# Kernel tuning notes

Measured on AMD Instinct MI355X. Metric: run time of the kernel, lower is better.

Reference implementation:

```python
import jax, jax.numpy as jnp
import numpy as np

BSZ, L, D = 64, 128, 2048


def setup_inputs() -> dict:
    key = jax.random.key(0)
    k1, k2, k3 = jax.random.split(key, 3)
    encoder_output = jax.random.normal(k1, (BSZ, L, D), dtype=jnp.float32)
    # ragged turn lengths in [2, L]; prefix mask like torch turn_lengths = mask.sum(1)
    lengths = jax.random.randint(k2, (BSZ,), 2, L + 1)
    mask = (jnp.arange(L)[None, :] < lengths[:, None]).astype(jnp.int32)
    W = jax.random.normal(k3, (2 * D, 2), dtype=jnp.float32) * (1.0 / np.sqrt(2 * D))
    b = jnp.zeros((2,), dtype=jnp.float32)
    return {"encoder_output": encoder_output, "mask": mask, "W": W, "b": b}


def reference(encoder_output, mask, W, b):
    bsz, max_len, d = encoder_output.shape
    turn_lengths = jnp.sum(mask, axis=1)  # [bsz]
    # con_fc(concat(h_j, h_k)) == h_j @ W[:d] + h_k @ W[d:] + b  (exact split of the linear)
    left = jnp.einsum('bld,dc->blc', encoder_output, W[:d])   # [b, L, 2]
    right = jnp.einsum('bld,dc->blc', encoder_output, W[d:])  # [b, L, 2]
    logits = left[:, :, None, :] + right[:, None, :, :] + b   # [b, L(j), L(k), 2]
    j = jnp.arange(max_len)[:, None]
    k = jnp.arange(max_len)[None, :]
    # pairs gathered by torch loops: k < j < turn_lengths[i]; label 1 iff k == j-1
    valid = (k < j) & (j < turn_lengths[:, None, None])        # [b, L, L]
    labels = (k == j - 1).astype(jnp.int32)                    # [L, L]
    logp = jax.nn.log_softmax(logits, axis=-1)                 # [b, L, L, 2]
    nll = -jnp.take_along_axis(
        logp, jnp.broadcast_to(labels[None, :, :, None], (bsz, max_len, max_len, 1)), axis=-1
    )[..., 0]                                                  # [b, L, L]
    n_valid = jnp.sum(valid)
    dli_loss = jnp.sum(jnp.where(valid, nll, 0.0)) / jnp.maximum(n_valid, 1).astype(nll.dtype)
    return dli_loss
```

## Files before the change

### kernel.cpp

```cpp
#include <hip/hip_runtime.h>

#define BSZ 64
#define LMAX 128
#define DIM 2048

struct Ctrl {
    float accum;
    int   count;
    int   done2;
};

__global__ __launch_bounds__(512) void proj_kernel(
        const float* __restrict__ enc,
        const float* __restrict__ W,
        float* __restrict__ proj,
        Ctrl* __restrict__ ctrl) {
    if (blockIdx.x == 0 && threadIdx.x == 0) {
        ctrl->accum = 0.0f;
        ctrl->count = 0;
        ctrl->done2 = 0;
    }

    __shared__ float4 sW[4][512];

    const float4* __restrict__ W4 = (const float4*)W;
    {
        const int i = threadIdx.x;
        sW[0][i] = W4[i * 2];
        sW[1][i] = W4[i * 2 + 1];
        sW[2][i] = W4[1024 + i * 2];
        sW[3][i] = W4[1024 + i * 2 + 1];
    }
    __syncthreads();

    const int wid  = threadIdx.x >> 6;
    const int lane = threadIdx.x & 63;
    const int p    = blockIdx.x * 8 + wid;

    const float4* __restrict__ h4 = (const float4*)(enc + (size_t)p * DIM);

    float a0 = 0.f, a1 = 0.f, a2 = 0.f, a3 = 0.f;
    #pragma unroll
    for (int it = 0; it < 8; ++it) {
        const int idx = it * 64 + lane;
        const float4 h  = h4[idx];
        const float4 w0 = sW[0][idx];
        const float4 w1 = sW[1][idx];
        const float4 w2 = sW[2][idx];
        const float4 w3 = sW[3][idx];
        a0 += h.x * w0.x + h.y * w0.z + h.z * w1.x + h.w * w1.z;
        a1 += h.x * w0.y + h.y * w0.w + h.z * w1.y + h.w * w1.w;
        a2 += h.x * w2.x + h.y * w2.z + h.z * w3.x + h.w * w3.z;
        a3 += h.x * w2.y + h.y * w2.w + h.z * w3.y + h.w * w3.w;
    }
    #pragma unroll
    for (int off = 32; off >= 1; off >>= 1) {
        a0 += __shfl_xor(a0, off);
        a1 += __shfl_xor(a1, off);
        a2 += __shfl_xor(a2, off);
        a3 += __shfl_xor(a3, off);
    }
    if (lane == 0) {
        float4 v; v.x = a0; v.y = a1; v.z = a2; v.w = a3;
        ((float4*)proj)[p] = v;
    }
}

__global__ __launch_bounds__(256) void loss_kernel(
        const int* __restrict__ mask,
        const float* __restrict__ proj,
        const float* __restrict__ bias,
        Ctrl* __restrict__ ctrl,
        float* __restrict__ out) {
    __shared__ float4 s_proj[LMAX];
    __shared__ float  s_w[4];
    __shared__ int    s_m[4];

    const int b   = blockIdx.x >> 2;
    const int q   = blockIdx.x & 3;
    const int tid = threadIdx.x;

    if (tid < LMAX) s_proj[tid] = ((const float4*)proj)[b * LMAX + tid];

    int m = (tid < LMAX) ? mask[b * LMAX + tid] : 0;
    #pragma unroll
    for (int off = 32; off >= 1; off >>= 1) m += __shfl_xor(m, off);
    if ((tid & 63) == 0) s_m[tid >> 6] = m;
    __syncthreads();

    const int   T  = s_m[0] + s_m[1] + s_m[2] + s_m[3];
    const float b0 = bias[0];
    const float b1 = bias[1];

    float local = 0.f;
    const int tmax = T << 7;
    for (int t = q * 256 + tid; t < tmax; t += 1024) {
        const int j = t >> 7;
        const int k = t & (LMAX - 1);
        if (k < j) {
            const float4 pj = s_proj[j];
            const float4 pk = s_proj[k];
            const float l0 = pj.x + pk.z + b0;
            const float l1 = pj.y + pk.w + b1;
            const bool  pos = (k == j - 1);
            const float d  = pos ? (l0 - l1) : (l1 - l0);
            local += fmaxf(d, 0.f) + __logf(1.f + __expf(-fabsf(d)));
        }
    }

    #pragma unroll
    for (int off = 32; off >= 1; off >>= 1) local += __shfl_xor(local, off);
    if ((tid & 63) == 0) s_w[tid >> 6] = local;
    __syncthreads();

    if (tid == 0) {
        atomicAdd(&ctrl->accum, s_w[0] + s_w[1] + s_w[2] + s_w[3]);
        if (q == 0) atomicAdd(&ctrl->count, T * (T - 1) / 2);
        __threadfence();
        const int prev = atomicAdd(&ctrl->done2, 1);
        if (prev == 4 * BSZ - 1) {
            const float s = atomicAdd(&ctrl->accum, 0.0f);
            const int   c = atomicAdd(&ctrl->count, 0);
            out[0] = s / (float)(c > 1 ? c : 1);
        }
    }
}

extern "C" void kernel_launch(void* const* d_in, const int* in_sizes, int n_in,
                              void* d_out, int out_size, void* d_ws, size_t ws_size,
                              hipStream_t stream) {
    const float* enc  = (const float*)d_in[0];
    const int*   mask = (const int*)d_in[1];
    const float* W    = (const float*)d_in[2];
    const float* bias = (const float*)d_in[3];
    float* out = (float*)d_out;

    float* proj = (float*)d_ws;
    Ctrl*  ctrl = (Ctrl*)((char*)d_ws + BSZ * LMAX * 16);

    proj_kernel<<<(BSZ * LMAX) / 8, 512, 0, stream>>>(enc, W, proj, ctrl);
    loss_kernel<<<4 * BSZ, 256, 0, stream>>>(mask, proj, bias, ctrl, out);
}
```

Before: 28.48 us.

## Keep W slices in registers, split rows across wave pairs, prefetch rows

The projection kernel no longer stages W in shared memory. Each wave holds half of W in registers and processes four consecutive rows, with the next row's loads issued before the current row's FMAs run. Each row is split across two waves that write separate partial results, which the loss kernel adds together. A transpose-style shuffle reduction is meant to cut shuffle count. In exchange the kernel uses more registers, launches half as many blocks, and needs twice the workspace for partials.

```diff
diff --git a/kernel.cpp b/kernel.cpp
--- a/kernel.cpp
+++ b/kernel.cpp
@@ -3,6 +3,7 @@
 #define BSZ 64
 #define LMAX 128
 #define DIM 2048
+#define NPOS (BSZ * LMAX)
 
 struct Ctrl {
     float accum;
@@ -10,59 +11,82 @@
     int   done2;
 };
 
-__global__ __launch_bounds__(512) void proj_kernel(
+__global__ __launch_bounds__(512, 4) void proj_kernel(
         const float* __restrict__ enc,
         const float* __restrict__ W,
         float* __restrict__ proj,
         Ctrl* __restrict__ ctrl) {
     if (blockIdx.x == 0 && threadIdx.x == 0) {
-        ctrl->accum = 0.0f;
-        ctrl->count = 0;
-        ctrl->done2 = 0;
+        ctrl->accum = 0.f; ctrl->count = 0; ctrl->done2 = 0;
     }
 
-    __shared__ float4 sW[4][512];
+    const int tid  = threadIdx.x;
+    const int wid  = tid >> 6;
+    const int lane = tid & 63;
+    const int pair = wid >> 1;
+    const int half = wid & 1;
+    const int p0   = blockIdx.x * 16 + pair * 4;
 
     const float4* __restrict__ W4 = (const float4*)W;
-    {
-        const int i = threadIdx.x;
-        sW[0][i] = W4[i * 2];
-        sW[1][i] = W4[i * 2 + 1];
-        sW[2][i] = W4[1024 + i * 2];
-        sW[3][i] = W4[1024 + i * 2 + 1];
+    float4 wl0[4], wl1[4], wr0[4], wr1[4];
+    #pragma unroll
+    for (int it = 0; it < 4; ++it) {
+        const int idx = half * 256 + it * 64 + lane;
+        wl0[it] = W4[idx * 2];
+        wl1[it] = W4[idx * 2 + 1];
+        wr0[it] = W4[1024 + idx * 2];
+        wr1[it] = W4[1024 + idx * 2 + 1];
     }
-    __syncthreads();
 
-    const int wid  = threadIdx.x >> 6;
-    const int lane = threadIdx.x & 63;
-    const int p    = blockIdx.x * 8 + wid;
+    float a0[4], a1[4], a2[4], a3[4];
+    #pragma unroll
+    for (int q = 0; q < 4; ++q) { a0[q] = a1[q] = a2[q] = a3[q] = 0.f; }
 
-    const float4* __restrict__ h4 = (const float4*)(enc + (size_t)p * DIM);
+    const float4* __restrict__ h4 = (const float4*)enc;
+    const size_t base = (size_t)p0 * (DIM / 4) + half * 256 + lane;
 
-    float a0 = 0.f, a1 = 0.f, a2 = 0.f, a3 = 0.f;
+    float4 hq[4];
     #pragma unroll
-    for (int it = 0; it < 8; ++it) {
-        const int idx = it * 64 + lane;
-        const float4 h  = h4[idx];
-        const float4 w0 = sW[0][idx];
-        const float4 w1 = sW[1][idx];
-        const float4 w2 = sW[2][idx];
-        const float4 w3 = sW[3][idx];
-        a0 += h.x * w0.x + h.y * w0.z + h.z * w1.x + h.w * w1.z;
-        a1 += h.x * w0.y + h.y * w0.w + h.z * w1.y + h.w * w1.w;
-        a2 += h.x * w2.x + h.y * w2.z + h.z * w3.x + h.w * w3.z;
-        a3 += h.x * w2.y + h.y * w2.w + h.z * w3.y + h.w * w3.w;
+    for (int it = 0; it < 4; ++it) hq[it] = h4[base + it * 64];
+
+    #pragma unroll
+    for (int q = 0; q < 4; ++q) {
+        float4 hn[4];
+        if (q < 3) {
+            #pragma unroll
+            for (int it = 0; it < 4; ++it)
+                hn[it] = h4[base + (size_t)(q + 1) * (DIM / 4) + it * 64];
+        }
+        #pragma unroll
+        for (int it = 0; it < 4; ++it) {
+            const float4 h = hq[it];
+            a0[q] += h.x * wl0[it].x + h.y * wl0[it].z + h.z * wl1[it].x + h.w * wl1[it].z;
+            a1[q] += h.x * wl0[it].y + h.y * wl0[it].w + h.z * wl1[it].y + h.w * wl1[it].w;
+            a2[q] += h.x * wr0[it].x + h.y * wr0[it].z + h.z * wr1[it].x + h.w * wr1[it].z;
+            a3[q] += h.x * wr0[it].y + h.y * wr0[it].w + h.z * wr1[it].y + h.w * wr1[it].w;
+        }
+        if (q < 3) {
+            #pragma unroll
+            for (int it = 0; it < 4; ++it) hq[it] = hn[it];
+        }
     }
+
+    float* __restrict__ projf = proj + (size_t)half * NPOS * 4;
     #pragma unroll
-    for (int off = 32; off >= 1; off >>= 1) {
-        a0 += __shfl_xor(a0, off);
-        a1 += __shfl_xor(a1, off);
-        a2 += __shfl_xor(a2, off);
-        a3 += __shfl_xor(a3, off);
-    }
-    if (lane == 0) {
-        float4 v; v.x = a0; v.y = a1; v.z = a2; v.w = a3;
-        ((float4*)proj)[p] = v;
+    for (int q = 0; q < 4; ++q) {
+        const bool o1 = (lane & 1);
+        const float r1 = __shfl_xor(o1 ? a0[q] : a1[q], 1);
+        float s = (o1 ? a1[q] : a0[q]) + r1;
+        const float r2 = __shfl_xor(o1 ? a2[q] : a3[q], 1);
+        float t = (o1 ? a3[q] : a2[q]) + r2;
+        const bool o2 = (lane & 2);
+        const float r3 = __shfl_xor(o2 ? s : t, 2);
+        float u = (o2 ? t : s) + r3;
+        u += __shfl_xor(u, 4);
+        u += __shfl_xor(u, 8);
+        u += __shfl_xor(u, 16);
+        u += __shfl_xor(u, 32);
+        if (lane < 4) projf[(size_t)(p0 + q) * 4 + lane] = u;
     }
 }
 
@@ -80,7 +104,15 @@
     const int q   = blockIdx.x & 3;
     const int tid = threadIdx.x;
 
-    if (tid < LMAX) s_proj[tid] = ((const float4*)proj)[b * LMAX + tid];
+    const float4* proj4 = (const float4*)proj;
+    if (tid < LMAX) {
+        const float4 pa = proj4[b * LMAX + tid];
+        const float4 pb = proj4[NPOS + b * LMAX + tid];
+        float4 v;
+        v.x = pa.x + pb.x; v.y = pa.y + pb.y;
+        v.z = pa.z + pb.z; v.w = pa.w + pb.w;
+        s_proj[tid] = v;
+    }
 
     int m = (tid < LMAX) ? mask[b * LMAX + tid] : 0;
     #pragma unroll
@@ -136,8 +168,8 @@
     float* out = (float*)d_out;
 
     float* proj = (float*)d_ws;
-    Ctrl*  ctrl = (Ctrl*)((char*)d_ws + BSZ * LMAX * 16);
+    Ctrl*  ctrl = (Ctrl*)((char*)d_ws + 2 * NPOS * 16);
 
-    proj_kernel<<<(BSZ * LMAX) / 8, 512, 0, stream>>>(enc, W, proj, ctrl);
+    proj_kernel<<<NPOS / 16, 512, 0, stream>>>(enc, W, proj, ctrl);
     loss_kernel<<<4 * BSZ, 256, 0, stream>>>(mask, proj, bias, ctrl, out);
 }
```

Result: faster. 27.42 us (-3.7%).
